# Kernel tuning notes

Measured on AMD Instinct MI355X. Metric: run time of the kernel, lower is better.

## Reference

```python
import jax, jax.numpy as jnp
import numpy as np

D_MODEL = 1024
HEADS = 16
D_K = D_MODEL // HEADS
D_FF = 4096
EPS = 1e-6


def setup_inputs() -> dict:
    key = jax.random.key(0)
    ks = jax.random.split(key, 20)
    B, S, D = 8, 1024, D_MODEL
    sc = 1.0 / np.sqrt(D)
    scf = 1.0 / np.sqrt(D_FF)
    inp = {
        "x": jax.random.normal(ks[0], (B, S, D), jnp.float32),
        "mask": jnp.ones((B, 1, 1, S), jnp.int32),
        "wq": jax.random.normal(ks[1], (D, D), jnp.float32) * sc,
        "bq": jnp.zeros((D,), jnp.float32),
        "wk": jax.random.normal(ks[2], (D, D), jnp.float32) * sc,
        "bk": jnp.zeros((D,), jnp.float32),
        "wv": jax.random.normal(ks[3], (D, D), jnp.float32) * sc,
        "bv": jnp.zeros((D,), jnp.float32),
        "wo": jax.random.normal(ks[4], (D, D), jnp.float32) * sc,
        "bo": jnp.zeros((D,), jnp.float32),
        "w1": jax.random.normal(ks[5], (D_FF, D), jnp.float32) * sc,
        "b1": jnp.zeros((D_FF,), jnp.float32),
        "w2": jax.random.normal(ks[6], (D, D_FF), jnp.float32) * scf,
        "b2": jnp.zeros((D,), jnp.float32),
        "g1": jnp.ones((D,), jnp.float32),
        "be1": jnp.zeros((D,), jnp.float32),
        "g2": jnp.ones((D,), jnp.float32),
        "be2": jnp.zeros((D,), jnp.float32),
    }
    return inp


def _layernorm(x, gamma, beta):
    # Faithful to custom LayerNorm: unbiased std (ddof=1), divide by (std+eps)
    mean = jnp.mean(x, axis=-1, keepdims=True)
    std = jnp.std(x, axis=-1, ddof=1, keepdims=True)
    return gamma * (x - mean) / (std + EPS) + beta


def _mha(x, mask, wq, bq, wk, bk, wv, bv, wo, bo):
    B, S, D = x.shape
    q = x @ wq.T + bq
    k = x @ wk.T + bk
    v = x @ wv.T + bv
    # [B,S,D] -> [B,H,S,dk]
    q = q.reshape(B, S, HEADS, D_K).transpose(0, 2, 1, 3)
    k = k.reshape(B, S, HEADS, D_K).transpose(0, 2, 1, 3)
    v = v.reshape(B, S, HEADS, D_K).transpose(0, 2, 1, 3)
    scores = jnp.einsum("bhqd,bhkd->bhqk", q, k) / np.sqrt(D_K).astype(np.float32)
    scores = jnp.where(mask == 0, jnp.float32(-1e9), scores)
    attn = jax.nn.softmax(scores, axis=-1)
    out = jnp.einsum("bhqk,bhkd->bhqd", attn, v)
    out = out.transpose(0, 2, 1, 3).reshape(B, S, D)
    return out @ wo.T + bo


def reference(x, mask, wq, bq, wk, bk, wv, bv, wo, bo, w1, b1, w2, b2, g1, be1, g2, be2):
    # residual 1: x + MHA(LN(x))
    h = _layernorm(x, g1, be1)
    x = x + _mha(h, mask, wq, bq, wk, bk, wv, bv, wo, bo)
    # residual 2: x + FFN(LN(x))
    h = _layernorm(x, g2, be2)
    ff = jax.nn.relu(h @ w1.T + b1) @ w2.T + b2
    return x + ff
```

## Files before the change

kernel.cpp:

```cpp
#include <hip/hip_runtime.h>

typedef __attribute__((ext_vector_type(8))) short short8;
typedef __attribute__((ext_vector_type(4))) short short4_t;
typedef __attribute__((ext_vector_type(4))) float floatx4;
typedef __attribute__((ext_vector_type(16))) float floatx16;

#define NTOK 8192
#define S_ 1024
#define DM 1024

__device__ __forceinline__ unsigned short f2b(float f) {
    union { float f; unsigned u; } v; v.f = f;
    unsigned r = v.u + 0x7FFF + ((v.u >> 16) & 1);
    return (unsigned short)(r >> 16);
}

__device__ __forceinline__ void gl_lds16(const void* g, void* l) {
    __builtin_amdgcn_global_load_lds((const __attribute__((address_space(1))) void*)g,
                                     (__attribute__((address_space(3))) void*)l, 16, 0, 0);
}

__global__ __launch_bounds__(256) void prep_kernel(const float* __restrict__ wq,
                                                   const float* __restrict__ wk,
                                                   const float* __restrict__ wv,
                                                   const float* __restrict__ wo,
                                                   const float* __restrict__ w1,
                                                   const float* __restrict__ w2,
                                                   const float* __restrict__ bq,
                                                   const float* __restrict__ bk,
                                                   const float* __restrict__ bv,
                                                   const int* __restrict__ mask,
                                                   unsigned short* __restrict__ wqkv_bf,
                                                   unsigned short* __restrict__ wo_bf,
                                                   unsigned short* __restrict__ w1_bf,
                                                   unsigned short* __restrict__ w2_bf,
                                                   float* __restrict__ bqkv,
                                                   float* __restrict__ mbias,
                                                   int* __restrict__ mflags) {
    const int bid = blockIdx.x;
    const int t = threadIdx.x;
    if (bid < 12288) {
        const int q = bid * 256 + t;
        const float* src;
        unsigned short* dst;
        int lq;
        if (q < 786432) {
            src = (q < 262144) ? wq : (q < 524288 ? wk : wv);
            lq = q & 262143;
            dst = wqkv_bf + (size_t)(q >> 18) * 1048576;
        } else if (q < 1048576) {
            src = wo; lq = q - 786432; dst = wo_bf;
        } else if (q < 2097152) {
            src = w1; lq = q - 1048576; dst = w1_bf;
        } else {
            src = w2; lq = q - 2097152; dst = w2_bf;
        }
        const float4 v = *reinterpret_cast<const float4*>(src + (size_t)lq * 4);
        short4_t o;
        o.x = (short)f2b(v.x); o.y = (short)f2b(v.y);
        o.z = (short)f2b(v.z); o.w = (short)f2b(v.w);
        *reinterpret_cast<short4_t*>(dst + (size_t)lq * 4) = o;
        return;
    }
    if (bid == 12288) {
#pragma unroll
        for (int it = 0; it < 3; ++it) {
            const int q = t + it * 256;
            const float* src = (q < 256) ? bq : (q < 512 ? bk : bv);
            const int lq = q & 255;
            *reinterpret_cast<float4*>(bqkv + q * 4) =
                *reinterpret_cast<const float4*>(src + lq * 4);
        }
        return;
    }
#pragma unroll
    for (int it = 0; it < 8; ++it) {
        const int q = t + it * 256;
        const int4 m = *reinterpret_cast<const int4*>(mask + q * 4);
        float4 o;
        o.x = (m.x == 0) ? -1e9f : 0.f;
        o.y = (m.y == 0) ? -1e9f : 0.f;
        o.z = (m.z == 0) ? -1e9f : 0.f;
        o.w = (m.w == 0) ? -1e9f : 0.f;
        *reinterpret_cast<float4*>(mbias + q * 4) = o;
    }
    if (t < 128) {
        int f = 0;
        const int* mp = mask + t * 64;
#pragma unroll
        for (int k = 0; k < 64; ++k) f |= (mp[k] == 0) ? 1 : 0;
        mflags[t] = f;
    }
}

__global__ __launch_bounds__(256) void ln_kernel(const float* __restrict__ x,
                                                 const float* __restrict__ g,
                                                 const float* __restrict__ be,
                                                 unsigned short* __restrict__ out) {
    const int row = blockIdx.x;
    const int t = threadIdx.x;
    const float4 xv = *reinterpret_cast<const float4*>(x + (size_t)row * DM + t * 4);
    float s = xv.x + xv.y + xv.z + xv.w;
#pragma unroll
    for (int off = 32; off > 0; off >>= 1) s += __shfl_down(s, off);
    __shared__ float red[8];
    const int wid = t >> 6, lane = t & 63;
    if (lane == 0) red[wid] = s;
    __syncthreads();
    const float mean = (red[0] + red[1] + red[2] + red[3]) * (1.f / 1024.f);
    const float dx = xv.x - mean, dy = xv.y - mean, dz = xv.z - mean, dw = xv.w - mean;
    float ss = dx * dx + dy * dy + dz * dz + dw * dw;
#pragma unroll
    for (int off = 32; off > 0; off >>= 1) ss += __shfl_down(ss, off);
    if (lane == 0) red[4 + wid] = ss;
    __syncthreads();
    const float var = (red[4] + red[5] + red[6] + red[7]) * (1.f / 1023.f);
    const float inv = 1.f / (sqrtf(var) + 1e-6f);
    const float4 gv = *reinterpret_cast<const float4*>(g + t * 4);
    const float4 bv = *reinterpret_cast<const float4*>(be + t * 4);
    short4_t o;
    o.x = (short)f2b(gv.x * dx * inv + bv.x);
    o.y = (short)f2b(gv.y * dy * inv + bv.y);
    o.z = (short)f2b(gv.z * dz * inv + bv.z);
    o.w = (short)f2b(gv.w * dw * inv + bv.w);
    *reinterpret_cast<short4_t*>(out + (size_t)row * DM + t * 4) = o;
}

template <int EPI>
__global__ __launch_bounds__(256, 2) void gemm_bt(const unsigned short* __restrict__ A,
                                                  const unsigned short* __restrict__ Bm,
                                                  const float* __restrict__ bias,
                                                  const float* __restrict__ res,
                                                  void* __restrict__ outp,
                                                  int M, int N, int K, int tilesX) {
    __shared__ __align__(16) unsigned short lds[2][2][8192];
    const int t = threadIdx.x;
    const int lane = t & 63, wid = t >> 6;
    const int wr = wid >> 1, wc = wid & 1;

    const int bid = blockIdx.x;
    const int xcd = bid & 7;
    const int lid = bid >> 3;
    const int sid = lid >> 5;
    const int off = lid & 31;
    const int gsid = sid * 8 + xcd;
    const int supercols = tilesX >> 2;
    const int srow = gsid / supercols;
    const int scol = gsid - srow * supercols;
    const int rowBase = (srow * 8 + (off >> 2)) * 128;
    const int colBase = (scol * 4 + (off & 3)) * 128;

    const int NT = K >> 6;
    const int lr31 = lane & 31;
    const int kh = lane >> 5;

    const unsigned short* Ag[4];
    const unsigned short* Bg[4];
#pragma unroll
    for (int j = 0; j < 4; ++j) {
        const int L = j * 256 + t;
        const int r = L >> 3;
        const int c = ((L & 7) ^ (r & 7)) * 8;
        Ag[j] = A + (size_t)(rowBase + r) * K + c;
        Bg[j] = Bm + (size_t)(colBase + r) * K + c;
    }

    floatx16 acc[2][2] = {};

#pragma unroll
    for (int j = 0; j < 4; ++j) gl_lds16(Ag[j], &lds[0][0][j * 2048 + wid * 512]);
#pragma unroll
    for (int j = 0; j < 4; ++j) gl_lds16(Bg[j], &lds[0][1][j * 2048 + wid * 512]);
#pragma unroll
    for (int j = 0; j < 4; ++j) { Ag[j] += 64; Bg[j] += 64; }

    int cur = 0;
    for (int tt = 0; tt < NT; ++tt) {
        if (tt + 1 < NT) {
#pragma unroll
            for (int j = 0; j < 4; ++j)
                gl_lds16(Ag[j], &lds[cur ^ 1][0][j * 2048 + wid * 512]);
#pragma unroll
            for (int j = 0; j < 4; ++j)
                gl_lds16(Bg[j], &lds[cur ^ 1][1][j * 2048 + wid * 512]);
#pragma unroll
            for (int j = 0; j < 4; ++j) { Ag[j] += 64; Bg[j] += 64; }
            asm volatile("s_waitcnt vmcnt(8)" ::: "memory");
        } else {
            asm volatile("s_waitcnt vmcnt(0)" ::: "memory");
        }
        __builtin_amdgcn_s_barrier();
        __builtin_amdgcn_sched_barrier(0);
        const unsigned short* Ab = &lds[cur][0][0];
        const unsigned short* Bb = &lds[cur][1][0];
#pragma unroll
        for (int ks = 0; ks < 4; ++ks) {
            short8 af[2], bfr[2];
#pragma unroll
            for (int mf = 0; mf < 2; ++mf) {
                const int r = wr * 64 + mf * 32 + lr31;
                const int cp = (ks * 2 + kh) ^ (r & 7);
                af[mf] = *reinterpret_cast<const short8*>(&Ab[r * 64 + cp * 8]);
            }
#pragma unroll
            for (int nf = 0; nf < 2; ++nf) {
                const int r = wc * 64 + nf * 32 + lr31;
                const int cp = (ks * 2 + kh) ^ (r & 7);
                bfr[nf] = *reinterpret_cast<const short8*>(&Bb[r * 64 + cp * 8]);
            }
            __builtin_amdgcn_s_setprio(1);
#pragma unroll
            for (int mf = 0; mf < 2; ++mf)
#pragma unroll
                for (int nf = 0; nf < 2; ++nf)
                    acc[mf][nf] = __builtin_amdgcn_mfma_f32_32x32x16_bf16(af[mf], bfr[nf], acc[mf][nf], 0, 0, 0);
            __builtin_amdgcn_s_setprio(0);
        }
        __builtin_amdgcn_sched_barrier(0);
        __builtin_amdgcn_s_barrier();
        cur ^= 1;
    }

    const int rbw = rowBase + wr * 64;
    const int cbw = colBase + wc * 64;
    const int lc31 = lane & 31;
    if (EPI == 4) {
        unsigned short* qh = (unsigned short*)outp;
        const float SC2 = 0.18033688f;
#pragma unroll
        for (int nf = 0; nf < 2; ++nf) {
            const int c = cbw + nf * 32 + lc31;
            const float bn = bias[c];
            const int sect = c >> 10;
            const int hh = (c >> 6) & 15;
            const int dd = c & 63;
            const float scl = (sect == 0) ? SC2 : 1.f;
#pragma unroll
            for (int mf = 0; mf < 2; ++mf) {
#pragma unroll
                for (int rg = 0; rg < 4; ++rg) {
                    const int r0 = rbw + mf * 32 + rg * 8 + 4 * kh;
                    const int bb = r0 >> 10, ss = r0 & 1023;
                    if (sect == 2) {
                        short4_t pk;
#pragma unroll
                        for (int j = 0; j < 4; ++j) pk[j] = (short)f2b(acc[mf][nf][rg * 4 + j] + bn);
                        *reinterpret_cast<short4_t*>(
                            &qh[16777216 + ((size_t)((bb * 16 + hh) * 64 + dd)) * 1024 + ss]) = pk;
                    } else {
                        unsigned short* base = qh + sect * 8388608;
#pragma unroll
                        for (int j = 0; j < 4; ++j)
                            base[((size_t)((bb * 16 + hh) * 1024 + ss + j)) * 64 + dd] =
                                f2b((acc[mf][nf][rg * 4 + j] + bn) * scl);
                    }
                }
            }
        }
        return;
    }
#pragma unroll
    for (int nf = 0; nf < 2; ++nf) {
        const int c = cbw + nf * 32 + lc31;
        const float bn = bias[c];
#pragma unroll
        for (int mf = 0; mf < 2; ++mf) {
#pragma unroll
            for (int rg = 0; rg < 4; ++rg) {
#pragma unroll
                for (int j = 0; j < 4; ++j) {
                    const int r = rbw + mf * 32 + rg * 8 + 4 * kh + j;
                    ((float*)outp)[(size_t)r * N + c] =
                        acc[mf][nf][rg * 4 + j] + bn + res[(size_t)r * N + c];
                }
            }
        }
    }
}

__global__ __launch_bounds__(512, 2) void gemm256p(const unsigned short* __restrict__ A,
                                                   const unsigned short* __restrict__ Bm,
                                                   const float* __restrict__ bias,
                                                   unsigned short* __restrict__ outp,
                                                   int M, int N, int K, int tilesX) {
    __shared__ __align__(16) unsigned short Abuf[2][16384];
    __shared__ __align__(16) unsigned short Bbuf[2][16384];
    const int t = threadIdx.x;
    const int lane = t & 63, wid = t >> 6;
    const int wr = wid >> 2, wc = wid & 3;

    const int bid = blockIdx.x;
    const int xcd = bid & 7;
    const int lid = bid >> 3;
    const int sid = lid >> 5;
    const int off = lid & 31;
    const int gsid = sid * 8 + xcd;
    const int supercols = tilesX >> 2;
    const int srow = gsid / supercols;
    const int scol = gsid - srow * supercols;
    const int rowBase = (srow * 8 + (off >> 2)) * 256;
    const int colBase = (scol * 4 + (off & 3)) * 256;

    const int NT = K >> 6;
    const int lr31 = lane & 31;
    const int kh = lane >> 5;
    const int x7 = lane & 7;

    const int rho_s = t >> 3;
    const int csrc = ((t & 7) ^ (rho_s & 7)) * 8;
    const int ldst = t * 8;
    const unsigned short* Bs_[2][2];
    const unsigned short* As_[2][2];
#pragma unroll
    for (int h = 0; h < 2; ++h)
#pragma unroll
        for (int j = 0; j < 2; ++j) {
            const int rr = rho_s + j * 64;
            Bs_[h][j] = Bm + (size_t)(colBase + h * 128 + rr) * K + csrc;
            As_[h][j] = A + (size_t)(rowBase + ((rr >> 6) * 128 + h * 64 + (rr & 63))) * K + csrc;
        }

#define STG_BH(h_, b_, kk_)                                                   \
    do {                                                                      \
        gl_lds16(Bs_[h_][0] + (kk_), &Bbuf[b_][(h_)*8192 + ldst]);            \
        gl_lds16(Bs_[h_][1] + (kk_), &Bbuf[b_][(h_)*8192 + 4096 + ldst]);     \
    } while (0)
#define STG_AH(h_, b_, kk_)                                                   \
    do {                                                                      \
        gl_lds16(As_[h_][0] + (kk_), &Abuf[b_][(h_)*8192 + ldst]);            \
        gl_lds16(As_[h_][1] + (kk_), &Abuf[b_][(h_)*8192 + 4096 + ldst]);     \
    } while (0)

    floatx16 acc[4][2] = {};

    STG_BH(0, 0, 0); STG_BH(1, 0, 0); STG_AH(0, 0, 0); STG_AH(1, 0, 0);
    asm volatile("s_waitcnt vmcnt(0)" ::: "memory");
    __builtin_amdgcn_s_barrier();

    for (int kt = 0; kt < NT; ++kt) {
        const int cur = kt & 1, nxt = cur ^ 1;
        const bool pf = (kt + 1 < NT);
        const int kkn = (pf ? kt + 1 : kt) << 6;
        short8 bfr[2][4];
#pragma unroll
        for (int q = 0; q < 4; ++q) {
            short8 af[4];
            {
                const int rho = wr * 64 + (q & 1) * 32 + lr31;
                const unsigned short* Ab = &Abuf[cur][(q >> 1) * 8192];
#pragma unroll
                for (int s = 0; s < 4; ++s)
                    af[s] = *reinterpret_cast<const short8*>(
                        &Ab[rho * 64 + ((2 * s + kh) ^ x7) * 8]);
            }
            if (q == 0) {
#pragma unroll
                for (int nf = 0; nf < 2; ++nf) {
                    const int gcol = wc * 64 + nf * 32 + lr31;
                    const unsigned short* Bb = &Bbuf[cur][(gcol >> 7) * 8192];
                    const int rho = gcol & 127;
#pragma unroll
                    for (int s = 0; s < 4; ++s)
                        bfr[nf][s] = *reinterpret_cast<const short8*>(
                            &Bb[rho * 64 + ((2 * s + kh) ^ x7) * 8]);
                }
            }
            if (pf) {
                if (q == 0) STG_BH(0, nxt, kkn);
                if (q == 1) STG_BH(1, nxt, kkn);
                if (q == 2) STG_AH(0, nxt, kkn);
                if (q == 3) STG_AH(1, nxt, kkn);
            }
            __builtin_amdgcn_s_barrier();
            asm volatile("s_waitcnt lgkmcnt(0)" ::: "memory");
            __builtin_amdgcn_sched_barrier(0);
            __builtin_amdgcn_s_setprio(1);
#pragma unroll
            for (int s = 0; s < 4; ++s)
#pragma unroll
                for (int nf = 0; nf < 2; ++nf)
                    acc[q][nf] = __builtin_amdgcn_mfma_f32_32x32x16_bf16(af[s], bfr[nf][s], acc[q][nf], 0, 0, 0);
            __builtin_amdgcn_s_setprio(0);
            __builtin_amdgcn_sched_barrier(0);
            if (q == 1) {
                if (pf) asm volatile("s_waitcnt vmcnt(4)" ::: "memory");
                else    asm volatile("s_waitcnt vmcnt(0)" ::: "memory");
            }
            if (q == 3 && pf) asm volatile("s_waitcnt vmcnt(2)" ::: "memory");
            __builtin_amdgcn_s_barrier();
        }
    }
#undef STG_AH
#undef STG_BH

    const int rbw = rowBase + wr * 128;
    const int cbw = colBase + wc * 64;
    const int lc31 = lane & 31;
#pragma unroll
    for (int nf = 0; nf < 2; ++nf) {
        const int c = cbw + nf * 32 + lc31;
        const float bn = bias[c];
#pragma unroll
        for (int q = 0; q < 4; ++q) {
#pragma unroll
            for (int rg = 0; rg < 4; ++rg) {
                const int r0 = rbw + q * 32 + rg * 8 + 4 * kh;
#pragma unroll
                for (int j = 0; j < 4; ++j) {
                    const float v = fmaxf(acc[q][nf][rg * 4 + j] + bn, 0.f);
                    outp[(size_t)(r0 + j) * N + c] = f2b(v);
                }
            }
        }
    }
}

__global__ __launch_bounds__(256) void attn_mfma(const unsigned short* __restrict__ Qh,
                                                 const unsigned short* __restrict__ Kh,
                                                 const unsigned short* __restrict__ Vt,
                                                 const float* __restrict__ mbias,
                                                 const int* __restrict__ mflags,
                                                 unsigned short* __restrict__ out) {
    __shared__ __align__(16) unsigned short Kbuf[2][4096];
    __shared__ __align__(16) unsigned short Vbuf[2][4096];
    __shared__ __align__(16) unsigned short Pbuf[4][16][72];
    __shared__ __align__(16) float mk[1024];
    const int t = threadIdx.x;
    const int w = t >> 6, l = t & 63;
    const int g = l >> 4, q16 = l & 15;
    const int x7 = q16 & 7;
    const int bid = blockIdx.x;
    const int swz = (bid & 7) * 256 + (bid >> 3);
    const int bh = swz >> 4, qb = swz & 15;
    const int b = bh >> 4, h = bh & 15;

    const size_t qbase = ((size_t)bh * 1024 + qb * 64 + w * 16 + q16) * 64;
    const short8 qf0 = *reinterpret_cast<const short8*>(Qh + qbase + g * 8);
    const short8 qf1 = *reinterpret_cast<const short8*>(Qh + qbase + 32 + g * 8);

    const int r0 = t >> 3;
    const int c0 = ((t & 7) ^ (r0 & 7)) * 8;
    const unsigned short* Kg = Kh + (size_t)bh * 65536 + r0 * 64 + c0;
    const unsigned short* Vg = Vt + (size_t)bh * 65536 + r0 * 1024 + c0;

#define ATTN_STAGE(bi, kc_)                                                        \
    do {                                                                           \
        gl_lds16(Kg + (kc_) * 4096, &Kbuf[bi][w * 512]);                           \
        gl_lds16(Kg + (kc_) * 4096 + 2048, &Kbuf[bi][2048 + w * 512]);             \
        gl_lds16(Vg + (kc_) * 64, &Vbuf[bi][w * 512]);                             \
        gl_lds16(Vg + (kc_) * 64 + 32768, &Vbuf[bi][2048 + w * 512]);              \
    } while (0)

    gl_lds16(mbias + b * 1024 + t * 4, &mk[w * 256]);
    ATTN_STAGE(0, 0);

    floatx4 oacc[4] = {};
    floatx4 loacc = {};
    short8 ones;
#pragma unroll
    for (int j = 0; j < 8; ++j) ones[j] = (short)0x3F80;

    int cur = 0;
    for (int kc = 0; kc < 16; ++kc) {
        if (kc < 15) {
            ATTN_STAGE(cur ^ 1, kc + 1);
            asm volatile("s_waitcnt vmcnt(4)" ::: "memory");
        } else {
            asm volatile("s_waitcnt vmcnt(0)" ::: "memory");
        }
        __builtin_amdgcn_s_barrier();
        __builtin_amdgcn_sched_barrier(0);
        const unsigned short* Kb = Kbuf[cur];
        const unsigned short* Vb = Vbuf[cur];

        floatx4 st[4] = {};
        __builtin_amdgcn_s_setprio(1);
#pragma unroll
        for (int t4 = 0; t4 < 4; ++t4) {
            const int row = t4 * 16 + q16;
            const short8 kf0 = *reinterpret_cast<const short8*>(&Kb[row * 64 + (g ^ x7) * 8]);
            const short8 kf1 = *reinterpret_cast<const short8*>(&Kb[row * 64 + ((4 + g) ^ x7) * 8]);
            st[t4] = __builtin_amdgcn_mfma_f32_16x16x32_bf16(kf0, qf0, st[t4], 0, 0, 0);
            st[t4] = __builtin_amdgcn_mfma_f32_16x16x32_bf16(kf1, qf1, st[t4], 0, 0, 0);
        }
        __builtin_amdgcn_s_setprio(0);

        if (mflags[b * 16 + kc]) {
#pragma unroll
            for (int t4 = 0; t4 < 4; ++t4) {
                const float4 mbv = *reinterpret_cast<const float4*>(&mk[kc * 64 + t4 * 16 + g * 4]);
#pragma unroll
                for (int r = 0; r < 4; ++r) st[t4][r] += ((const float*)&mbv)[r];
            }
        }
#pragma unroll
        for (int t4 = 0; t4 < 4; ++t4) {
            const float p0 = __builtin_exp2f(st[t4][0]);
            const float p1 = __builtin_exp2f(st[t4][1]);
            const float p2 = __builtin_exp2f(st[t4][2]);
            const float p3 = __builtin_exp2f(st[t4][3]);
            unsigned u0, u1;
            asm("v_cvt_pk_bf16_f32 %0, %1, %2" : "=v"(u0) : "v"(p0), "v"(p1));
            asm("v_cvt_pk_bf16_f32 %0, %1, %2" : "=v"(u1) : "v"(p2), "v"(p3));
            uint2 pr; pr.x = u0; pr.y = u1;
            *reinterpret_cast<uint2*>(&Pbuf[w][q16][t4 * 16 + g * 4]) = pr;
        }

        const short8 pf0 = *reinterpret_cast<const short8*>(&Pbuf[w][q16][g * 8]);
        const short8 pf1 = *reinterpret_cast<const short8*>(&Pbuf[w][q16][32 + g * 8]);
        __builtin_amdgcn_s_setprio(1);
        loacc = __builtin_amdgcn_mfma_f32_16x16x32_bf16(pf0, ones, loacc, 0, 0, 0);
        loacc = __builtin_amdgcn_mfma_f32_16x16x32_bf16(pf1, ones, loacc, 0, 0, 0);
#pragma unroll
        for (int n = 0; n < 4; ++n) {
            const int row = n * 16 + q16;
            const short8 vf0 = *reinterpret_cast<const short8*>(&Vb[row * 64 + (g ^ x7) * 8]);
            const short8 vf1 = *reinterpret_cast<const short8*>(&Vb[row * 64 + ((4 + g) ^ x7) * 8]);
            oacc[n] = __builtin_amdgcn_mfma_f32_16x16x32_bf16(pf0, vf0, oacc[n], 0, 0, 0);
            oacc[n] = __builtin_amdgcn_mfma_f32_16x16x32_bf16(pf1, vf1, oacc[n], 0, 0, 0);
        }
        __builtin_amdgcn_s_setprio(0);
        __builtin_amdgcn_sched_barrier(0);
        __builtin_amdgcn_s_barrier();
        cur ^= 1;
    }
#undef ATTN_STAGE

    const size_t obase = ((size_t)b * S_ + qb * 64 + w * 16) * 1024 + h * 64;
#pragma unroll
    for (int r = 0; r < 4; ++r) {
        const float invr = 1.f / loacc[r];
        const size_t orow = obase + (size_t)(g * 4 + r) * 1024;
#pragma unroll
        for (int n = 0; n < 4; ++n)
            out[orow + n * 16 + q16] = f2b(oacc[n][r] * invr);
    }
}

extern "C" void kernel_launch(void* const* d_in, const int* in_sizes, int n_in,
                              void* d_out, int out_size, void* d_ws, size_t ws_size,
                              hipStream_t stream) {
    const float* x   = (const float*)d_in[0];
    const int*  mask = (const int*)d_in[1];
    const float* wq  = (const float*)d_in[2];
    const float* bq  = (const float*)d_in[3];
    const float* wk  = (const float*)d_in[4];
    const float* bk  = (const float*)d_in[5];
    const float* wv  = (const float*)d_in[6];
    const float* bv  = (const float*)d_in[7];
    const float* wo  = (const float*)d_in[8];
    const float* bo  = (const float*)d_in[9];
    const float* w1  = (const float*)d_in[10];
    const float* b1  = (const float*)d_in[11];
    const float* w2  = (const float*)d_in[12];
    const float* b2  = (const float*)d_in[13];
    const float* g1  = (const float*)d_in[14];
    const float* be1 = (const float*)d_in[15];
    const float* g2  = (const float*)d_in[16];
    const float* be2 = (const float*)d_in[17];

    char* ws = (char*)d_ws;
    unsigned short* wqkv_bf = (unsigned short*)(ws);
    unsigned short* wo_bf   = (unsigned short*)(ws + 6291456);
    unsigned short* w1_bf   = (unsigned short*)(ws + 8388608);
    unsigned short* w2_bf   = (unsigned short*)(ws + 16777216);
    float*          bqkv    = (float*)(ws + 25165824);
    float*          mbias   = (float*)(ws + 25178112);
    int*            mflags  = (int*)(ws + 25210880);
    unsigned short* h_bf    = (unsigned short*)(ws + 25214976);
    float*          x1      = (float*)(ws + 41992192);
    unsigned short* attn_bf = (unsigned short*)(ws + 75546624);
    unsigned short* qkvh    = (unsigned short*)(ws + 92323840);
    unsigned short* ff1_bf  = (unsigned short*)(ws + 92323840);

    prep_kernel<<<12290, 256, 0, stream>>>(wq, wk, wv, wo, w1, w2, bq, bk, bv, mask,
                                           wqkv_bf, wo_bf, w1_bf, w2_bf, bqkv, mbias, mflags);

    ln_kernel<<<NTOK, 256, 0, stream>>>(x, g1, be1, h_bf);
    gemm_bt<4><<<24 * 64, 256, 0, stream>>>(h_bf, wqkv_bf, bqkv, nullptr, qkvh, NTOK, 3072, 1024, 24);
    attn_mfma<<<2048, 256, 0, stream>>>(qkvh, qkvh + 8388608, qkvh + 16777216, mbias, mflags, attn_bf);
    gemm_bt<1><<<8 * 64, 256, 0, stream>>>(attn_bf, wo_bf, bo, x, x1, NTOK, 1024, 1024, 8);
    ln_kernel<<<NTOK, 256, 0, stream>>>(x1, g2, be2, h_bf);
    gemm256p<<<512, 512, 0, stream>>>(h_bf, w1_bf, b1, ff1_bf, NTOK, 4096, 1024, 16);
    gemm_bt<1><<<8 * 64, 256, 0, stream>>>(ff1_bf, w2_bf, b2, x1, (float*)d_out, NTOK, 1024, 4096, 8);
}
```

Before: 362.8 us.

## Store residual x1 in bf16 and fuse the first LayerNorm into the prep kernel

The first LayerNorm is folded into the weight-conversion prep kernel as extra blocks, which removes one kernel launch. The intermediate residual x1 is now written as bf16 instead of fp32 by the output-projection GEMM epilogue. A new bf16-input LayerNorm reads it, and the final FFN GEMM adds it back as bf16. This cuts memory traffic for the residual stream in exchange for reduced precision in the residual path.

```diff
diff --git a/kernel.cpp b/kernel.cpp
--- a/kernel.cpp
+++ b/kernel.cpp
@@ -13,6 +13,11 @@
     union { float f; unsigned u; } v; v.f = f;
     unsigned r = v.u + 0x7FFF + ((v.u >> 16) & 1);
     return (unsigned short)(r >> 16);
+}
+
+__device__ __forceinline__ float b2f(unsigned short u) {
+    union { unsigned u; float f; } v; v.u = ((unsigned)u) << 16;
+    return v.f;
 }
 
 __device__ __forceinline__ void gl_lds16(const void* g, void* l) {
@@ -30,13 +35,17 @@
                                                    const float* __restrict__ bk,
                                                    const float* __restrict__ bv,
                                                    const int* __restrict__ mask,
+                                                   const float* __restrict__ x,
+                                                   const float* __restrict__ g1,
+                                                   const float* __restrict__ be1,
                                                    unsigned short* __restrict__ wqkv_bf,
                                                    unsigned short* __restrict__ wo_bf,
                                                    unsigned short* __restrict__ w1_bf,
                                                    unsigned short* __restrict__ w2_bf,
                                                    float* __restrict__ bqkv,
                                                    float* __restrict__ mbias,
-                                                   int* __restrict__ mflags) {
+                                                   int* __restrict__ mflags,
+                                                   unsigned short* __restrict__ h_bf) {
     const int bid = blockIdx.x;
     const int t = threadIdx.x;
     if (bid < 12288) {
@@ -73,32 +82,28 @@
         }
         return;
     }
-#pragma unroll
-    for (int it = 0; it < 8; ++it) {
-        const int q = t + it * 256;
-        const int4 m = *reinterpret_cast<const int4*>(mask + q * 4);
-        float4 o;
-        o.x = (m.x == 0) ? -1e9f : 0.f;
-        o.y = (m.y == 0) ? -1e9f : 0.f;
-        o.z = (m.z == 0) ? -1e9f : 0.f;
-        o.w = (m.w == 0) ? -1e9f : 0.f;
-        *reinterpret_cast<float4*>(mbias + q * 4) = o;
-    }
-    if (t < 128) {
-        int f = 0;
-        const int* mp = mask + t * 64;
-#pragma unroll
-        for (int k = 0; k < 64; ++k) f |= (mp[k] == 0) ? 1 : 0;
-        mflags[t] = f;
-    }
-}
-
-__global__ __launch_bounds__(256) void ln_kernel(const float* __restrict__ x,
-                                                 const float* __restrict__ g,
-                                                 const float* __restrict__ be,
-                                                 unsigned short* __restrict__ out) {
-    const int row = blockIdx.x;
-    const int t = threadIdx.x;
+    if (bid == 12289) {
+#pragma unroll
+        for (int it = 0; it < 8; ++it) {
+            const int q = t + it * 256;
+            const int4 m = *reinterpret_cast<const int4*>(mask + q * 4);
+            float4 o;
+            o.x = (m.x == 0) ? -1e9f : 0.f;
+            o.y = (m.y == 0) ? -1e9f : 0.f;
+            o.z = (m.z == 0) ? -1e9f : 0.f;
+            o.w = (m.w == 0) ? -1e9f : 0.f;
+            *reinterpret_cast<float4*>(mbias + q * 4) = o;
+        }
+        if (t < 128) {
+            int f = 0;
+            const int* mp = mask + t * 64;
+#pragma unroll
+            for (int k = 0; k < 64; ++k) f |= (mp[k] == 0) ? 1 : 0;
+            mflags[t] = f;
+        }
+        return;
+    }
+    const int row = bid - 12290;
     const float4 xv = *reinterpret_cast<const float4*>(x + (size_t)row * DM + t * 4);
     float s = xv.x + xv.y + xv.z + xv.w;
 #pragma unroll
@@ -116,13 +121,51 @@
     __syncthreads();
     const float var = (red[4] + red[5] + red[6] + red[7]) * (1.f / 1023.f);
     const float inv = 1.f / (sqrtf(var) + 1e-6f);
+    const float4 gv = *reinterpret_cast<const float4*>(g1 + t * 4);
+    const float4 bev = *reinterpret_cast<const float4*>(be1 + t * 4);
+    short4_t o;
+    o.x = (short)f2b(gv.x * dx * inv + bev.x);
+    o.y = (short)f2b(gv.y * dy * inv + bev.y);
+    o.z = (short)f2b(gv.z * dz * inv + bev.z);
+    o.w = (short)f2b(gv.w * dw * inv + bev.w);
+    *reinterpret_cast<short4_t*>(h_bf + (size_t)row * DM + t * 4) = o;
+}
+
+__global__ __launch_bounds__(256) void ln_bf16(const unsigned short* __restrict__ xb,
+                                               const float* __restrict__ g,
+                                               const float* __restrict__ be,
+                                               unsigned short* __restrict__ out) {
+    const int row = blockIdx.x;
+    const int t = threadIdx.x;
+    const short4_t xv4 = *reinterpret_cast<const short4_t*>(xb + (size_t)row * DM + t * 4);
+    float xv[4];
+#pragma unroll
+    for (int j = 0; j < 4; ++j) xv[j] = b2f((unsigned short)xv4[j]);
+    float s = xv[0] + xv[1] + xv[2] + xv[3];
+#pragma unroll
+    for (int off = 32; off > 0; off >>= 1) s += __shfl_down(s, off);
+    __shared__ float red[8];
+    const int wid = t >> 6, lane = t & 63;
+    if (lane == 0) red[wid] = s;
+    __syncthreads();
+    const float mean = (red[0] + red[1] + red[2] + red[3]) * (1.f / 1024.f);
+    float d[4];
+#pragma unroll
+    for (int j = 0; j < 4; ++j) d[j] = xv[j] - mean;
+    float ss = d[0] * d[0] + d[1] * d[1] + d[2] * d[2] + d[3] * d[3];
+#pragma unroll
+    for (int off = 32; off > 0; off >>= 1) ss += __shfl_down(ss, off);
+    if (lane == 0) red[4 + wid] = ss;
+    __syncthreads();
+    const float var = (red[4] + red[5] + red[6] + red[7]) * (1.f / 1023.f);
+    const float inv = 1.f / (sqrtf(var) + 1e-6f);
     const float4 gv = *reinterpret_cast<const float4*>(g + t * 4);
-    const float4 bv = *reinterpret_cast<const float4*>(be + t * 4);
+    const float4 bev = *reinterpret_cast<const float4*>(be + t * 4);
     short4_t o;
-    o.x = (short)f2b(gv.x * dx * inv + bv.x);
-    o.y = (short)f2b(gv.y * dy * inv + bv.y);
-    o.z = (short)f2b(gv.z * dz * inv + bv.z);
-    o.w = (short)f2b(gv.w * dw * inv + bv.w);
+    o.x = (short)f2b(gv.x * d[0] * inv + bev.x);
+    o.y = (short)f2b(gv.y * d[1] * inv + bev.y);
+    o.z = (short)f2b(gv.z * d[2] * inv + bev.z);
+    o.w = (short)f2b(gv.w * d[3] * inv + bev.w);
     *reinterpret_cast<short4_t*>(out + (size_t)row * DM + t * 4) = o;
 }
 
@@ -130,7 +173,7 @@
 __global__ __launch_bounds__(256, 2) void gemm_bt(const unsigned short* __restrict__ A,
                                                   const unsigned short* __restrict__ Bm,
                                                   const float* __restrict__ bias,
-                                                  const float* __restrict__ res,
+                                                  const void* __restrict__ res,
                                                   void* __restrict__ outp,
                                                   int M, int N, int K, int tilesX) {
     __shared__ __align__(16) unsigned short lds[2][2][8192];
@@ -270,8 +313,15 @@
 #pragma unroll
                 for (int j = 0; j < 4; ++j) {
                     const int r = rbw + mf * 32 + rg * 8 + 4 * kh + j;
-                    ((float*)outp)[(size_t)r * N + c] =
-                        acc[mf][nf][rg * 4 + j] + bn + res[(size_t)r * N + c];
+                    if (EPI == 2) {
+                        const float v = acc[mf][nf][rg * 4 + j] + bn +
+                                        ((const float*)res)[(size_t)r * N + c];
+                        ((unsigned short*)outp)[(size_t)r * N + c] = f2b(v);
+                    } else {
+                        const float v = acc[mf][nf][rg * 4 + j] + bn +
+                                        b2f(((const unsigned short*)res)[(size_t)r * N + c]);
+                        ((float*)outp)[(size_t)r * N + c] = v;
+                    }
                 }
             }
         }
@@ -568,19 +618,19 @@
     float*          mbias   = (float*)(ws + 25178112);
     int*            mflags  = (int*)(ws + 25210880);
     unsigned short* h_bf    = (unsigned short*)(ws + 25214976);
-    float*          x1      = (float*)(ws + 41992192);
+    unsigned short* x1b     = (unsigned short*)(ws + 41992192);
     unsigned short* attn_bf = (unsigned short*)(ws + 75546624);
     unsigned short* qkvh    = (unsigned short*)(ws + 92323840);
     unsigned short* ff1_bf  = (unsigned short*)(ws + 92323840);
 
-    prep_kernel<<<12290, 256, 0, stream>>>(wq, wk, wv, wo, w1, w2, bq, bk, bv, mask,
-                                           wqkv_bf, wo_bf, w1_bf, w2_bf, bqkv, mbias, mflags);
-
-    ln_kernel<<<NTOK, 256, 0, stream>>>(x, g1, be1, h_bf);
+    prep_kernel<<<20482, 256, 0, stream>>>(wq, wk, wv, wo, w1, w2, bq, bk, bv, mask,
+                                           x, g1, be1,
+                                           wqkv_bf, wo_bf, w1_bf, w2_bf, bqkv, mbias, mflags, h_bf);
+
     gemm_bt<4><<<24 * 64, 256, 0, stream>>>(h_bf, wqkv_bf, bqkv, nullptr, qkvh, NTOK, 3072, 1024, 24);
     attn_mfma<<<2048, 256, 0, stream>>>(qkvh, qkvh + 8388608, qkvh + 16777216, mbias, mflags, attn_bf);
-    gemm_bt<1><<<8 * 64, 256, 0, stream>>>(attn_bf, wo_bf, bo, x, x1, NTOK, 1024, 1024, 8);
-    ln_kernel<<<NTOK, 256, 0, stream>>>(x1, g2, be2, h_bf);
+    gemm_bt<2><<<8 * 64, 256, 0, stream>>>(attn_bf, wo_bf, bo, x, x1b, NTOK, 1024, 1024, 8);
+    ln_bf16<<<NTOK, 256, 0, stream>>>(x1b, g2, be2, h_bf);
     gemm256p<<<512, 512, 0, stream>>>(h_bf, w1_bf, b1, ff1_bf, NTOK, 4096, 1024, 16);
-    gemm_bt<1><<<8 * 64, 256, 0, stream>>>(ff1_bf, w2_bf, b2, x1, (float*)d_out, NTOK, 1024, 4096, 8);
-}
+    gemm_bt<5><<<8 * 64, 256, 0, stream>>>(ff1_bf, w2_bf, b2, x1b, (float*)d_out, NTOK, 1024, 4096, 8);
+}
```

Result: no change. 356.2 us (median of 2 runs) (-1.8%).
